# Kernel optimization log

Hardware: AMD Instinct MI355X
Metric: run time of the kernel (lower is better)

Reference implementation:

```python
import jax, jax.numpy as jnp
from jax import lax
import numpy as np

B_SZ, L, NH, DH, DS = 2, 2048, 24, 64, 128


def setup_inputs() -> dict:
    key = jax.random.key(0)
    k1, k2, k3, k4 = jax.random.split(key, 4)
    x = jax.random.normal(k1, (B_SZ, L, NH, DH), dtype=jnp.float32)
    A = jax.random.normal(k2, (B_SZ, L, NH), dtype=jnp.float32)
    B_mat = jax.random.normal(k3, (B_SZ, L, NH, DS), dtype=jnp.float32)
    C_mat = jax.random.normal(k4, (B_SZ, L, NH, DS), dtype=jnp.float32)
    delta_param = jnp.zeros((NH,), dtype=jnp.float32)
    return {"x": x, "A": A, "B_mat": B_mat, "C_mat": C_mat, "delta_param": delta_param}


def reference(x, A, B_mat, C_mat, delta_param):
    # x: (B, L, nh, dh); A: (B, L, nh); B_mat/C_mat: (B, L, nh, ds)
    b, l, nh, dh = x.shape
    ds = B_mat.shape[-1]
    delta = jax.nn.softplus(A + delta_param[None, None, :])        # (B, L, nh)
    A_bar = jnp.exp(-delta * jnp.abs(A))                            # (B, L, nh)

    def step(h, inp):
        x_t, B_t, C_t, a_t = inp  # (B,nh,dh), (B,nh,ds), (B,nh,ds), (B,nh)
        h = a_t[:, :, None, None] * h + x_t[..., None] * B_t[:, :, None, :]
        y_t = jnp.einsum('bhds,bhs->bhd', h, C_t)                   # (B, nh, dh)
        return h, y_t

    h0 = jnp.zeros((b, nh, dh, ds), dtype=x.dtype)
    xs = (jnp.moveaxis(x, 1, 0),      # (L, B, nh, dh)
          jnp.moveaxis(B_mat, 1, 0),  # (L, B, nh, ds)
          jnp.moveaxis(C_mat, 1, 0),  # (L, B, nh, ds)
          jnp.moveaxis(A_bar, 1, 0))  # (L, B, nh)
    _, ys = lax.scan(step, h0, xs)    # ys: (L, B, nh, dh)
    return jnp.moveaxis(ys, 0, 1)     # (B, L, nh, dh)
```

## Files before the change

kernel.cpp:

```cpp
#include <hip/hip_runtime.h>

#define B_SZ 2
#define LSEQ 2048
#define NHh 24
#define DHh 64
#define DSs 128
#define TCH 64
#define NC  (LSEQ / TCH)
#define BH  (B_SZ * NHh)

#define S_ELEMS   (BH * LSEQ)
#define G_ELEMS   ((size_t)BH * NC * DSs * DHh)
#define WS_S_BYTES ((size_t)S_ELEMS * 4)
#define WS_G_BYTES (G_ELEMS * 2)
#define WS_REQ     (WS_S_BYTES + 2 * WS_G_BYTES)

#define SP  136
#define UP  72

typedef __attribute__((ext_vector_type(8))) short bf16x8;
typedef __attribute__((ext_vector_type(4))) float f32x4;

__device__ __forceinline__ unsigned short f2bf(float f) {
    union { float f; unsigned u; } v; v.f = f;
    unsigned r = ((v.u >> 16) & 1u) + 0x7FFFu;
    return (unsigned short)((v.u + r) >> 16);
}
__device__ __forceinline__ float bf2f(unsigned short h) {
    union { unsigned u; float f; } v; v.u = ((unsigned)h) << 16; return v.f;
}
__device__ __forceinline__ unsigned pk2(float a, float b) {
    return (unsigned)f2bf(a) | ((unsigned)f2bf(b) << 16);
}

__global__ __launch_bounds__(256, 2)
void k1_chunk(const float* __restrict__ x, const float* __restrict__ A,
              const float* __restrict__ Bm, const float* __restrict__ dp,
              float* __restrict__ S_ws, unsigned short* __restrict__ G_ws) {
    __shared__ __align__(16) unsigned short sBT[DSs][UP];
    __shared__ __align__(16) unsigned short sXT[DHh][UP];
    __shared__ float sF[TCH];

    const int c  = blockIdx.x & (NC - 1);
    const int bh = blockIdx.x >> 5;
    const int nh = bh % NHh; const int b = bh / NHh;
    const int tid = threadIdx.x;
    const int lane = tid & 63;
    const int w = tid >> 6;

    const size_t row0 = (size_t)(b * LSEQ + c * TCH) * NHh + nh;

    const int u = tid >> 2;
    const int q = tid & 3;
    const float* Brow = Bm + (row0 + (size_t)u * NHh) * DSs;
    const float* xrow = x  + (row0 + (size_t)u * NHh) * DHh;
    float4 bv[8], xv[4];
    #pragma unroll
    for (int j = 0; j < 8; ++j) bv[j] = *(const float4*)(Brow + (j * 4 + q) * 4);
    #pragma unroll
    for (int j = 0; j < 4; ++j) xv[j] = *(const float4*)(xrow + (j * 4 + q) * 4);

    if (tid < 64) {
        float a  = A[row0 + (size_t)tid * NHh];
        float z  = a + dp[nh];
        float sp = (z > 20.0f) ? z : log1pf(expf(z));
        float la = -sp * fabsf(a);
        #pragma unroll
        for (int off = 1; off < 64; off <<= 1) {
            float v = __shfl_up(la, off, 64);
            if (lane >= off) la += v;
        }
        S_ws[(size_t)bh * LSEQ + c * TCH + tid] = la;
        float s63 = __shfl(la, 63, 64);
        sF[tid] = expf(s63 - la);
    }
    __syncthreads();

    #pragma unroll
    for (int j = 0; j < 8; ++j) {
        const int s = (j * 4 + q) * 4;
        sBT[s + 0][u] = f2bf(bv[j].x);
        sBT[s + 1][u] = f2bf(bv[j].y);
        sBT[s + 2][u] = f2bf(bv[j].z);
        sBT[s + 3][u] = f2bf(bv[j].w);
    }
    const float f = sF[u];
    #pragma unroll
    for (int j = 0; j < 4; ++j) {
        const int d = (j * 4 + q) * 4;
        sXT[d + 0][u] = f2bf(xv[j].x * f);
        sXT[d + 1][u] = f2bf(xv[j].y * f);
        sXT[d + 2][u] = f2bf(xv[j].z * f);
        sXT[d + 3][u] = f2bf(xv[j].w * f);
    }
    __syncthreads();

    const int fr = lane >> 4, fc = lane & 15;
    bf16x8 afr0 = *(const bf16x8*)&sXT[16 * w + fc][fr * 8];
    bf16x8 afr1 = *(const bf16x8*)&sXT[16 * w + fc][32 + fr * 8];
    #pragma unroll
    for (int st = 0; st < 8; ++st) {
        f32x4 acc = {0.f, 0.f, 0.f, 0.f};
        bf16x8 b0 = *(const bf16x8*)&sBT[st * 16 + fc][fr * 8];
        bf16x8 b1 = *(const bf16x8*)&sBT[st * 16 + fc][32 + fr * 8];
        acc = __builtin_amdgcn_mfma_f32_16x16x32_bf16(afr0, b0, acc, 0, 0, 0);
        acc = __builtin_amdgcn_mfma_f32_16x16x32_bf16(afr1, b1, acc, 0, 0, 0);
        unsigned short* gout = G_ws +
            ((((size_t)bh * NC + c) * DHh + 16 * w + fr * 4) * DSs) + st * 16 + fc;
        #pragma unroll
        for (int r = 0; r < 4; ++r) gout[(size_t)r * DSs] = f2bf(acc[r]);
    }
}

__global__ __launch_bounds__(256)
void k2_scan(const float* __restrict__ S_ws, const unsigned short* __restrict__ G_ws,
             unsigned short* __restrict__ H_ws) {
    const int dblk = blockIdx.x & 3;
    const int bh   = blockIdx.x >> 2;
    const int tid  = threadIdx.x;
    const int d    = dblk * 16 + (tid >> 4);
    const int s0   = (tid & 15) * 8;

    float h[8];
    #pragma unroll
    for (int k = 0; k < 8; ++k) h[k] = 0.f;

    size_t base = (((size_t)bh * NC) * DHh + d) * DSs + s0;
    const size_t cstride = (size_t)DHh * DSs;

    uint4 gv = *(const uint4*)(G_ws + base);
    for (int c = 0; c < NC; ++c) {
        uint4 gn = (c + 1 < NC) ? *(const uint4*)(G_ws + base + (size_t)(c + 1) * cstride) : gv;
        const float e = expf(S_ws[(size_t)bh * LSEQ + c * TCH + (TCH - 1)]);
        uint4 p;
        p.x = pk2(h[0], h[1]); p.y = pk2(h[2], h[3]);
        p.z = pk2(h[4], h[5]); p.w = pk2(h[6], h[7]);
        *(uint4*)(H_ws + base + (size_t)c * cstride) = p;
        const unsigned gu[4] = {gv.x, gv.y, gv.z, gv.w};
        #pragma unroll
        for (int k = 0; k < 4; ++k) {
            h[2 * k]     = fmaf(e, h[2 * k],     bf2f((unsigned short)(gu[k] & 0xffff)));
            h[2 * k + 1] = fmaf(e, h[2 * k + 1], bf2f((unsigned short)(gu[k] >> 16)));
        }
        gv = gn;
    }
}

__global__ __launch_bounds__(256, 2)
void k3_y(const float* __restrict__ x, const float* __restrict__ Bm,
          const float* __restrict__ Cm, const float* __restrict__ S_ws,
          const unsigned short* __restrict__ H_ws, float* __restrict__ y) {
    __shared__ __align__(16) unsigned short sC[TCH][SP];
    __shared__ __align__(16) unsigned short sB[TCH][SP];
    __shared__ __align__(16) unsigned short sH[DHh][SP];
    __shared__ __align__(16) unsigned short sW[TCH][UP];
    __shared__ __align__(16) unsigned short sXT[DHh][UP];
    __shared__ float sS[TCH];
    __shared__ float sEt[TCH];

    const int c  = blockIdx.x & (NC - 1);
    const int bh = blockIdx.x >> 5;
    const int nh = bh % NHh; const int b = bh / NHh;
    const int tid = threadIdx.x;
    const int lane = tid & 63;
    const int w = tid >> 6;

    const size_t row0 = (size_t)(b * LSEQ + c * TCH) * NHh + nh;

    const int rr = tid >> 2;
    const int q  = tid & 3;
    const float* Crow = Cm + (row0 + (size_t)rr * NHh) * DSs;
    const float* Brow = Bm + (row0 + (size_t)rr * NHh) * DSs;
    const float* xrow = x  + (row0 + (size_t)rr * NHh) * DHh;
    const unsigned short* Hrow = H_ws + (((size_t)bh * NC + c) * DHh + rr) * DSs;
    float4 cv[8], bv[8], xv[4];
    uint4  hv[4];
    #pragma unroll
    for (int j = 0; j < 8; ++j) cv[j] = *(const float4*)(Crow + (j * 4 + q) * 4);
    #pragma unroll
    for (int j = 0; j < 8; ++j) bv[j] = *(const float4*)(Brow + (j * 4 + q) * 4);
    #pragma unroll
    for (int j = 0; j < 4; ++j) xv[j] = *(const float4*)(xrow + (j * 4 + q) * 4);
    #pragma unroll
    for (int j = 0; j < 4; ++j) hv[j] = *(const uint4*)(Hrow + (j * 4 + q) * 8);

    if (tid < 64) {
        float sv = S_ws[(size_t)bh * LSEQ + c * TCH + tid];
        sS[tid]  = sv;
        sEt[tid] = expf(sv);
    }

    #pragma unroll
    for (int j = 0; j < 8; ++j) {
        const int s = (j * 4 + q) * 4;
        *(uint2*)&sC[rr][s] = make_uint2(pk2(cv[j].x, cv[j].y), pk2(cv[j].z, cv[j].w));
        *(uint2*)&sB[rr][s] = make_uint2(pk2(bv[j].x, bv[j].y), pk2(bv[j].z, bv[j].w));
    }
    #pragma unroll
    for (int j = 0; j < 4; ++j)
        *(uint4*)&sH[rr][(j * 4 + q) * 8] = hv[j];
    #pragma unroll
    for (int j = 0; j < 4; ++j) {
        const int d = (j * 4 + q) * 4;
        sXT[d + 0][rr] = f2bf(xv[j].x);
        sXT[d + 1][rr] = f2bf(xv[j].y);
        sXT[d + 2][rr] = f2bf(xv[j].z);
        sXT[d + 3][rr] = f2bf(xv[j].w);
    }
    __syncthreads();

    const int fr = lane >> 4, fc = lane & 15;
    const int t0w = 16 * w;

    bf16x8 ca[4];
    #pragma unroll
    for (int kb = 0; kb < 4; ++kb)
        ca[kb] = *(const bf16x8*)&sC[t0w + fc][kb * 32 + fr * 8];
    float st4[4];
    #pragma unroll
    for (int r = 0; r < 4; ++r) st4[r] = sS[t0w + fr * 4 + r];

    #pragma unroll
    for (int ut = 0; ut < 4; ++ut) {
        const int u0 = ut * 16;
        unsigned short wv[4] = {0, 0, 0, 0};
        if (ut <= w) {
            f32x4 acc = {0.f, 0.f, 0.f, 0.f};
            #pragma unroll
            for (int kb = 0; kb < 4; ++kb) {
                bf16x8 bb = *(const bf16x8*)&sB[u0 + fc][kb * 32 + fr * 8];
                acc = __builtin_amdgcn_mfma_f32_16x16x32_bf16(ca[kb], bb, acc, 0, 0, 0);
            }
            const float su = sS[u0 + fc];
            const int   uu = u0 + fc;
            #pragma unroll
            for (int r = 0; r < 4; ++r) {
                const int t = t0w + fr * 4 + r;
                const float dd = fminf(st4[r] - su, 0.f);
                const float val = (uu <= t) ? acc[r] * expf(dd) : 0.f;
                wv[r] = f2bf(val);
            }
        }
        #pragma unroll
        for (int r = 0; r < 4; ++r) sW[t0w + fr * 4 + r][u0 + fc] = wv[r];
    }

    bf16x8 wa0 = *(const bf16x8*)&sW[t0w + fc][fr * 8];
    bf16x8 wa1;
    if (w >= 2) wa1 = *(const bf16x8*)&sW[t0w + fc][32 + fr * 8];
    float et4[4];
    #pragma unroll
    for (int r = 0; r < 4; ++r) et4[r] = sEt[t0w + fr * 4 + r];

    #pragma unroll
    for (int dt = 0; dt < 4; ++dt) {
        const int d0 = dt * 16;
        f32x4 acc = {0.f, 0.f, 0.f, 0.f};
        #pragma unroll
        for (int kb = 0; kb < 4; ++kb) {
            bf16x8 hb = *(const bf16x8*)&sH[d0 + fc][kb * 32 + fr * 8];
            acc = __builtin_amdgcn_mfma_f32_16x16x32_bf16(ca[kb], hb, acc, 0, 0, 0);
        }
        #pragma unroll
        for (int r = 0; r < 4; ++r) acc[r] *= et4[r];
        bf16x8 xb0 = *(const bf16x8*)&sXT[d0 + fc][fr * 8];
        acc = __builtin_amdgcn_mfma_f32_16x16x32_bf16(wa0, xb0, acc, 0, 0, 0);
        if (w >= 2) {
            bf16x8 xb1 = *(const bf16x8*)&sXT[d0 + fc][32 + fr * 8];
            acc = __builtin_amdgcn_mfma_f32_16x16x32_bf16(wa1, xb1, acc, 0, 0, 0);
        }
        float* yout = y + (row0 + (size_t)(t0w + fr * 4) * NHh) * DHh + d0 + fc;
        #pragma unroll
        for (int r = 0; r < 4; ++r) yout[(size_t)r * NHh * DHh] = acc[r];
    }
}

__device__ __forceinline__ void gload_lds16(const float* g, void* l) {
    __builtin_amdgcn_global_load_lds(
        (const __attribute__((address_space(1))) void*)g,
        (__attribute__((address_space(3))) void*)l, 16, 0, 0);
}
__device__ __forceinline__ void gload_lds4(const float* g, float* l) {
    __builtin_amdgcn_global_load_lds(
        (const __attribute__((address_space(1))) void*)g,
        (__attribute__((address_space(3))) void*)l, 4, 0, 0);
}
#define F_DBLK 4
#define F_DPW 16
#define F_TCH 32
#define F_NCH (LSEQ / F_TCH)
__global__ __launch_bounds__(256, 1)
void ssm_scan_fb(const float* __restrict__ x, const float* __restrict__ A,
                 const float* __restrict__ Bm, const float* __restrict__ Cm,
                 const float* __restrict__ dp, float* __restrict__ y) {
    __shared__ float s_abar[LSEQ];
    __shared__ float s_B[2][F_TCH][DSs];
    __shared__ float s_C[2][F_TCH][DSs];
    __shared__ float s_x[2][F_TCH][F_DPW];
    const int blk = blockIdx.x;
    const int dblk = blk % F_DBLK, bh = blk / F_DBLK;
    const int nh = bh % NHh, b = bh / NHh;
    const float dpv = dp[nh];
    for (int i = threadIdx.x; i < LSEQ; i += 256) {
        float a = A[(b * LSEQ + i) * NHh + nh];
        float z = a + dpv;
        float sp = (z > 20.0f) ? z : log1pf(expf(z));
        s_abar[i] = expf(-sp * fabsf(a));
    }
    const int tid = threadIdx.x, wid = tid >> 6, lane = tid & 63;
    const int dloc = tid >> 4, sg = tid & 15, sb = sg * 8;
    const size_t bh_off = (size_t)(b * LSEQ) * NHh + nh;
    const float* Bbase = Bm + bh_off * DSs;
    const float* Cbase = Cm + bh_off * DSs;
    const float* xbase = x + bh_off * DHh + dblk * F_DPW;
    float* yp = y + bh_off * DHh + dblk * F_DPW + dloc;
    const int RSTRIDE = NHh * DSs, XSTRIDE = NHh * DHh;
    auto stage = [&](int buf, int t0) {
        #pragma unroll
        for (int j = 0; j < 4; ++j) {
            const int r0 = (wid * 4 + j) * 2, r = r0 + (lane >> 5), col = (lane & 31) * 4;
            gload_lds16(Bbase + (size_t)(t0 + r) * RSTRIDE + col, &s_B[buf][r0][0]);
            gload_lds16(Cbase + (size_t)(t0 + r) * RSTRIDE + col, &s_C[buf][r0][0]);
        }
        #pragma unroll
        for (int j = 0; j < 2; ++j) {
            const int idx = (wid * 2 + j) * 64 + lane, t = idx >> 4, dc = idx & 15;
            gload_lds4(xbase + (size_t)(t0 + t) * XSTRIDE + dc, &s_x[buf][(wid * 2 + j) * 4][0]);
        }
    };
    stage(0, 0);
    __syncthreads();
    float h0=0,h1=0,h2=0,h3=0,h4=0,h5=0,h6=0,h7=0;
    for (int c = 0; c < F_NCH; ++c) {
        const int buf = c & 1;
        if (c + 1 < F_NCH) stage(buf ^ 1, (c + 1) * F_TCH);
        const int t0 = c * F_TCH;
        #pragma unroll 4
        for (int tt = 0; tt < F_TCH; ++tt) {
            const int t = t0 + tt;
            const float a = s_abar[t], xd = s_x[buf][tt][dloc];
            const float4* Br = (const float4*)&s_B[buf][tt][sb];
            const float4* Cr = (const float4*)&s_C[buf][tt][sb];
            const float4 B0 = Br[0], B1 = Br[1], C0 = Cr[0], C1 = Cr[1];
            h0 = fmaf(a, h0, xd * B0.x); h1 = fmaf(a, h1, xd * B0.y);
            h2 = fmaf(a, h2, xd * B0.z); h3 = fmaf(a, h3, xd * B0.w);
            h4 = fmaf(a, h4, xd * B1.x); h5 = fmaf(a, h5, xd * B1.y);
            h6 = fmaf(a, h6, xd * B1.z); h7 = fmaf(a, h7, xd * B1.w);
            float p0 = h0 * C0.x; p0 = fmaf(h1, C0.y, p0); p0 = fmaf(h2, C0.z, p0); p0 = fmaf(h3, C0.w, p0);
            float p1 = h4 * C1.x; p1 = fmaf(h5, C1.y, p1); p1 = fmaf(h6, C1.z, p1); p1 = fmaf(h7, C1.w, p1);
            float p = p0 + p1;
            p += __shfl_xor(p, 1, 64); p += __shfl_xor(p, 2, 64);
            p += __shfl_xor(p, 4, 64); p += __shfl_xor(p, 8, 64);
            if (sg == 0) yp[(size_t)t * XSTRIDE] = p;
        }
        __syncthreads();
    }
}

extern "C" void kernel_launch(void* const* d_in, const int* in_sizes, int n_in,
                              void* d_out, int out_size, void* d_ws, size_t ws_size,
                              hipStream_t stream) {
    const float* x  = (const float*)d_in[0];
    const float* A  = (const float*)d_in[1];
    const float* Bm = (const float*)d_in[2];
    const float* Cm = (const float*)d_in[3];
    const float* dp = (const float*)d_in[4];
    float* y = (float*)d_out;

    if (ws_size >= WS_REQ) {
        float* S_ws = (float*)d_ws;
        unsigned short* G_ws = (unsigned short*)((char*)d_ws + WS_S_BYTES);
        unsigned short* H_ws = G_ws + G_ELEMS;
        hipLaunchKernelGGL(k1_chunk, dim3(BH * NC), dim3(256), 0, stream,
                           x, A, Bm, dp, S_ws, G_ws);
        hipLaunchKernelGGL(k2_scan, dim3(BH * 4), dim3(256), 0, stream,
                           S_ws, G_ws, H_ws);
        hipLaunchKernelGGL(k3_y, dim3(BH * NC), dim3(256), 0, stream,
                           x, Bm, Cm, S_ws, H_ws, y);
    } else {
        hipLaunchKernelGGL(ssm_scan_fb, dim3(BH * F_DBLK), dim3(256), 0, stream,
                           x, A, Bm, Cm, dp, y);
    }
}
```

Before: 188.9 us.

## Load C and H fragments directly to registers, deepen scan prefetch, finer scan grid

k3 now loads C and H straight from global memory into MFMA register fragments instead of staging them through LDS. This shrinks shared memory per block and raises the occupancy hint to 3. k2 uses 64-thread blocks over 16 d-slices to spread across more CUs, with an 8-deep register prefetch of G and S to hide latency in the serial chunk scan. k1 moves the decay prefix computation after the B transpose and raises its occupancy hint. The direct fragment loads are less coalesced, and the larger register footprint may cap the intended occupancy.

```diff
diff --git a/kernel.cpp b/kernel.cpp
--- a/kernel.cpp
+++ b/kernel.cpp
@@ -33,7 +33,7 @@
     return (unsigned)f2bf(a) | ((unsigned)f2bf(b) << 16);
 }
 
-__global__ __launch_bounds__(256, 2)
+__global__ __launch_bounds__(256, 3)
 void k1_chunk(const float* __restrict__ x, const float* __restrict__ A,
               const float* __restrict__ Bm, const float* __restrict__ dp,
               float* __restrict__ S_ws, unsigned short* __restrict__ G_ws) {
@@ -60,22 +60,6 @@
     #pragma unroll
     for (int j = 0; j < 4; ++j) xv[j] = *(const float4*)(xrow + (j * 4 + q) * 4);
 
-    if (tid < 64) {
-        float a  = A[row0 + (size_t)tid * NHh];
-        float z  = a + dp[nh];
-        float sp = (z > 20.0f) ? z : log1pf(expf(z));
-        float la = -sp * fabsf(a);
-        #pragma unroll
-        for (int off = 1; off < 64; off <<= 1) {
-            float v = __shfl_up(la, off, 64);
-            if (lane >= off) la += v;
-        }
-        S_ws[(size_t)bh * LSEQ + c * TCH + tid] = la;
-        float s63 = __shfl(la, 63, 64);
-        sF[tid] = expf(s63 - la);
-    }
-    __syncthreads();
-
     #pragma unroll
     for (int j = 0; j < 8; ++j) {
         const int s = (j * 4 + q) * 4;
@@ -84,6 +68,23 @@
         sBT[s + 2][u] = f2bf(bv[j].z);
         sBT[s + 3][u] = f2bf(bv[j].w);
     }
+
+    if (tid < 64) {
+        float a  = A[row0 + (size_t)tid * NHh];
+        float z  = a + dp[nh];
+        float sp = (z > 20.0f) ? z : log1pf(expf(z));
+        float la = -sp * fabsf(a);
+        #pragma unroll
+        for (int off = 1; off < 64; off <<= 1) {
+            float v = __shfl_up(la, off, 64);
+            if (lane >= off) la += v;
+        }
+        S_ws[(size_t)bh * LSEQ + c * TCH + tid] = la;
+        float s63 = __shfl(la, 63, 64);
+        sF[tid] = expf(s63 - la);
+    }
+    __syncthreads();
+
     const float f = sF[u];
     #pragma unroll
     for (int j = 0; j < 4; ++j) {
@@ -112,13 +113,13 @@
     }
 }
 
-__global__ __launch_bounds__(256)
+__global__ __launch_bounds__(64)
 void k2_scan(const float* __restrict__ S_ws, const unsigned short* __restrict__ G_ws,
              unsigned short* __restrict__ H_ws) {
-    const int dblk = blockIdx.x & 3;
-    const int bh   = blockIdx.x >> 2;
+    const int dblk = blockIdx.x & 15;
+    const int bh   = blockIdx.x >> 4;
     const int tid  = threadIdx.x;
-    const int d    = dblk * 16 + (tid >> 4);
+    const int d    = dblk * 4 + (tid >> 4);
     const int s0   = (tid & 15) * 8;
 
     float h[8];
@@ -127,32 +128,43 @@
 
     size_t base = (((size_t)bh * NC) * DHh + d) * DSs + s0;
     const size_t cstride = (size_t)DHh * DSs;
-
-    uint4 gv = *(const uint4*)(G_ws + base);
-    for (int c = 0; c < NC; ++c) {
-        uint4 gn = (c + 1 < NC) ? *(const uint4*)(G_ws + base + (size_t)(c + 1) * cstride) : gv;
-        const float e = expf(S_ws[(size_t)bh * LSEQ + c * TCH + (TCH - 1)]);
-        uint4 p;
-        p.x = pk2(h[0], h[1]); p.y = pk2(h[2], h[3]);
-        p.z = pk2(h[4], h[5]); p.w = pk2(h[6], h[7]);
-        *(uint4*)(H_ws + base + (size_t)c * cstride) = p;
-        const unsigned gu[4] = {gv.x, gv.y, gv.z, gv.w};
-        #pragma unroll
-        for (int k = 0; k < 4; ++k) {
-            h[2 * k]     = fmaf(e, h[2 * k],     bf2f((unsigned short)(gu[k] & 0xffff)));
-            h[2 * k + 1] = fmaf(e, h[2 * k + 1], bf2f((unsigned short)(gu[k] >> 16)));
-        }
-        gv = gn;
-    }
-}
-
-__global__ __launch_bounds__(256, 2)
+    const float* Se = S_ws + (size_t)bh * LSEQ + (TCH - 1);
+
+    uint4 g[8]; float sv[8];
+    #pragma unroll
+    for (int j = 0; j < 8; ++j) {
+        g[j]  = *(const uint4*)(G_ws + base + (size_t)j * cstride);
+        sv[j] = Se[(size_t)j * TCH];
+    }
+    #pragma unroll
+    for (int c = 0; c < NC; c += 8) {
+        #pragma unroll
+        for (int j = 0; j < 8; ++j) {
+            const int cc = c + j;
+            uint4 p;
+            p.x = pk2(h[0], h[1]); p.y = pk2(h[2], h[3]);
+            p.z = pk2(h[4], h[5]); p.w = pk2(h[6], h[7]);
+            *(uint4*)(H_ws + base + (size_t)cc * cstride) = p;
+            const float e = expf(sv[j]);
+            const unsigned gu[4] = {g[j].x, g[j].y, g[j].z, g[j].w};
+            #pragma unroll
+            for (int k = 0; k < 4; ++k) {
+                h[2 * k]     = fmaf(e, h[2 * k],     bf2f((unsigned short)(gu[k] & 0xffff)));
+                h[2 * k + 1] = fmaf(e, h[2 * k + 1], bf2f((unsigned short)(gu[k] >> 16)));
+            }
+            if (cc + 8 < NC) {
+                g[j]  = *(const uint4*)(G_ws + base + (size_t)(cc + 8) * cstride);
+                sv[j] = Se[(size_t)(cc + 8) * TCH];
+            }
+        }
+    }
+}
+
+__global__ __launch_bounds__(256, 3)
 void k3_y(const float* __restrict__ x, const float* __restrict__ Bm,
           const float* __restrict__ Cm, const float* __restrict__ S_ws,
           const unsigned short* __restrict__ H_ws, float* __restrict__ y) {
-    __shared__ __align__(16) unsigned short sC[TCH][SP];
     __shared__ __align__(16) unsigned short sB[TCH][SP];
-    __shared__ __align__(16) unsigned short sH[DHh][SP];
     __shared__ __align__(16) unsigned short sW[TCH][UP];
     __shared__ __align__(16) unsigned short sXT[DHh][UP];
     __shared__ float sS[TCH];
@@ -164,41 +176,51 @@
     const int tid = threadIdx.x;
     const int lane = tid & 63;
     const int w = tid >> 6;
+    const int fr = lane >> 4, fc = lane & 15;
+    const int t0w = 16 * w;
 
     const size_t row0 = (size_t)(b * LSEQ + c * TCH) * NHh + nh;
 
     const int rr = tid >> 2;
     const int q  = tid & 3;
-    const float* Crow = Cm + (row0 + (size_t)rr * NHh) * DSs;
     const float* Brow = Bm + (row0 + (size_t)rr * NHh) * DSs;
     const float* xrow = x  + (row0 + (size_t)rr * NHh) * DHh;
-    const unsigned short* Hrow = H_ws + (((size_t)bh * NC + c) * DHh + rr) * DSs;
-    float4 cv[8], bv[8], xv[4];
-    uint4  hv[4];
-    #pragma unroll
-    for (int j = 0; j < 8; ++j) cv[j] = *(const float4*)(Crow + (j * 4 + q) * 4);
+    float4 bv[8], xv[4];
     #pragma unroll
     for (int j = 0; j < 8; ++j) bv[j] = *(const float4*)(Brow + (j * 4 + q) * 4);
     #pragma unroll
     for (int j = 0; j < 4; ++j) xv[j] = *(const float4*)(xrow + (j * 4 + q) * 4);
-    #pragma unroll
-    for (int j = 0; j < 4; ++j) hv[j] = *(const uint4*)(Hrow + (j * 4 + q) * 8);
+
+    const float* Cfr = Cm + (row0 + (size_t)(t0w + fc) * NHh) * DSs + fr * 8;
+    float4 cf[8];
+    #pragma unroll
+    for (int kb = 0; kb < 4; ++kb) {
+        cf[2 * kb]     = *(const float4*)(Cfr + kb * 32);
+        cf[2 * kb + 1] = *(const float4*)(Cfr + kb * 32 + 4);
+    }
 
     if (tid < 64) {
-        float sv = S_ws[(size_t)bh * LSEQ + c * TCH + tid];
-        sS[tid]  = sv;
-        sEt[tid] = expf(sv);
+        float svv = S_ws[(size_t)bh * LSEQ + c * TCH + tid];
+        sS[tid]  = svv;
+        sEt[tid] = expf(svv);
+    }
+
+    bf16x8 ca[4];
+    #pragma unroll
+    for (int kb = 0; kb < 4; ++kb) {
+        bf16x8 t;
+        t[0] = (short)f2bf(cf[2 * kb].x);     t[1] = (short)f2bf(cf[2 * kb].y);
+        t[2] = (short)f2bf(cf[2 * kb].z);     t[3] = (short)f2bf(cf[2 * kb].w);
+        t[4] = (short)f2bf(cf[2 * kb + 1].x); t[5] = (short)f2bf(cf[2 * kb + 1].y);
+        t[6] = (short)f2bf(cf[2 * kb + 1].z); t[7] = (short)f2bf(cf[2 * kb + 1].w);
+        ca[kb] = t;
     }
 
     #pragma unroll
     for (int j = 0; j < 8; ++j) {
         const int s = (j * 4 + q) * 4;
-        *(uint2*)&sC[rr][s] = make_uint2(pk2(cv[j].x, cv[j].y), pk2(cv[j].z, cv[j].w));
         *(uint2*)&sB[rr][s] = make_uint2(pk2(bv[j].x, bv[j].y), pk2(bv[j].z, bv[j].w));
     }
-    #pragma unroll
-    for (int j = 0; j < 4; ++j)
-        *(uint4*)&sH[rr][(j * 4 + q) * 8] = hv[j];
     #pragma unroll
     for (int j = 0; j < 4; ++j) {
         const int d = (j * 4 + q) * 4;
@@ -207,15 +229,18 @@
         sXT[d + 2][rr] = f2bf(xv[j].z);
         sXT[d + 3][rr] = f2bf(xv[j].w);
     }
+
+    const unsigned short* Hfr = H_ws + (((size_t)bh * NC + c) * DHh + fc) * DSs + fr * 8;
+    bf16x8 hf[4][4];
+    #pragma unroll
+    for (int dt = 0; dt < 4; ++dt) {
+        #pragma unroll
+        for (int kb = 0; kb < 4; ++kb)
+            hf[dt][kb] = *(const bf16x8*)(Hfr + (size_t)(dt * 16) * DSs + kb * 32);
+    }
+
     __syncthreads();
 
-    const int fr = lane >> 4, fc = lane & 15;
-    const int t0w = 16 * w;
-
-    bf16x8 ca[4];
-    #pragma unroll
-    for (int kb = 0; kb < 4; ++kb)
-        ca[kb] = *(const bf16x8*)&sC[t0w + fc][kb * 32 + fr * 8];
     float st4[4];
     #pragma unroll
     for (int r = 0; r < 4; ++r) st4[r] = sS[t0w + fr * 4 + r];
@@ -257,10 +282,8 @@
         const int d0 = dt * 16;
         f32x4 acc = {0.f, 0.f, 0.f, 0.f};
         #pragma unroll
-        for (int kb = 0; kb < 4; ++kb) {
-            bf16x8 hb = *(const bf16x8*)&sH[d0 + fc][kb * 32 + fr * 8];
-            acc = __builtin_amdgcn_mfma_f32_16x16x32_bf16(ca[kb], hb, acc, 0, 0, 0);
-        }
+        for (int kb = 0; kb < 4; ++kb)
+            acc = __builtin_amdgcn_mfma_f32_16x16x32_bf16(ca[kb], hf[dt][kb], acc, 0, 0, 0);
         #pragma unroll
         for (int r = 0; r < 4; ++r) acc[r] *= et4[r];
         bf16x8 xb0 = *(const bf16x8*)&sXT[d0 + fc][fr * 8];
@@ -373,7 +396,7 @@
         unsigned short* H_ws = G_ws + G_ELEMS;
         hipLaunchKernelGGL(k1_chunk, dim3(BH * NC), dim3(256), 0, stream,
                            x, A, Bm, dp, S_ws, G_ws);
-        hipLaunchKernelGGL(k2_scan, dim3(BH * 4), dim3(256), 0, stream,
+        hipLaunchKernelGGL(k2_scan, dim3(BH * 16), dim3(64), 0, stream,
                            S_ws, G_ws, H_ws);
         hipLaunchKernelGGL(k3_y, dim3(BH * NC), dim3(256), 0, stream,
                            x, Bm, Cm, S_ws, H_ws, y);
```

Measured after the change: 192.6 us. No clear change (+2.0%).
